# Kernel tuning notes

Measured on AMD Instinct MI355X. Metric: run time of the kernel, lower is better.

## Reference

```python
import jax, jax.numpy as jnp
import numpy as np

V, D, H, L = 50000, 50, 50, 100   # vocab, input_dim, hidden_dim, latent_dim
WIN = 5
B = 65536
MARGIN = 1.0


def setup_inputs() -> dict:
    key = jax.random.key(0)
    ks = jax.random.split(key, 12)
    emb = jax.random.normal(ks[0], (V, D), jnp.float32) * 0.1
    emb = emb.at[0].set(0.0)  # padding_idx=0
    W1 = jax.random.normal(ks[1], (2 * D, H), jnp.float32) * 0.1
    b1 = jnp.zeros((H,), jnp.float32)
    Wmu = jax.random.normal(ks[2], (H, L), jnp.float32) * 0.1
    bmu = jnp.zeros((L,), jnp.float32)
    Wls = jax.random.normal(ks[3], (H, 1), jnp.float32) * 0.1
    bls = jnp.zeros((1,), jnp.float32)
    type_means_tbl = jax.random.normal(ks[4], (V, L), jnp.float32) * 0.1
    type_logvars_tbl = jax.random.normal(ks[5], (V, 1), jnp.float32) * 0.1
    centers = jax.random.randint(ks[6], (B,), 1, V, jnp.int32)
    contexts = jax.random.randint(ks[7], (B, 2 * WIN), 1, V, jnp.int32)
    neg_contexts = jax.random.randint(ks[8], (B, 2 * WIN), 1, V, jnp.int32)
    return {"emb": emb, "W1": W1, "b1": b1, "Wmu": Wmu, "bmu": bmu,
            "Wls": Wls, "bls": bls, "type_means_tbl": type_means_tbl,
            "type_logvars_tbl": type_logvars_tbl, "centers": centers,
            "contexts": contexts, "neg_contexts": neg_contexts}


def _kl(idx, post_mu, post_logsigma, type_means_tbl, type_logvars_tbl):
    # idx: [N] int; post_mu: [N,L]; post_logsigma: [N,1]
    post_sigma = jnp.exp(post_logsigma)                      # [N,1]
    type_mean = type_means_tbl[idx]                          # [N,L]
    type_logvar = type_logvars_tbl[idx]                      # [N,1]
    type_var = jnp.exp(type_logvar)                          # [N,1]
    var_division = post_sigma / type_var                     # [N,1]
    diff = post_mu - type_mean                               # [N,L]
    diff_term = jnp.sum(diff * diff, axis=1, keepdims=True) / type_var  # [N,1]
    logvar_division = type_logvar - post_logsigma            # [N,1]
    return 0.5 * ((var_division + diff_term + logvar_division)[:, 0] - L)  # [N]


def reference(emb, W1, b1, Wmu, bmu, Wls, bls, type_means_tbl, type_logvars_tbl,
              centers, contexts, neg_contexts):
    Bn, C = contexts.shape                                   # C = 2*window
    e_ctx = emb[contexts]                                    # [B,C,D]
    e_cen = emb[centers]                                     # [B,D]
    # concat(context_embed, center_repeat) along feature dim -> [B,C,2D]
    cat = jnp.concatenate(
        [e_ctx, jnp.broadcast_to(e_cen[:, None, :], (Bn, C, D))], axis=-1)
    h = jax.nn.relu(jnp.einsum('bcf,fh->bch', cat, W1) + b1).sum(axis=1)  # [B,H]
    mu = h @ Wmu + bmu                                       # [B,L]
    logsigma = h @ Wls + bls                                 # [B,1]
    # repeat each row 2*window times (matches repeat(1,2w).view(-1,L))
    mus = jnp.repeat(mu, C, axis=0)                          # [B*C,L]
    logsigmas = jnp.repeat(logsigma, C, axis=0)              # [B*C,1]
    kl_ctx = _kl(contexts.reshape(-1), mus, logsigmas, type_means_tbl, type_logvars_tbl)
    kl_neg = _kl(neg_contexts.reshape(-1), mus, logsigmas, type_means_tbl, type_logvars_tbl)
    kl_cen = _kl(centers, mu, logsigma, type_means_tbl, type_logvars_tbl)
    hinge = jnp.maximum(kl_ctx - kl_neg + MARGIN, 0.0)
    loss = hinge.sum() + kl_cen.sum()
    return loss / Bn
```

## Files before the change

### kernel.cpp

```cpp
#include <hip/hip_runtime.h>

namespace {
constexpr int V    = 50000;
constexpr int D    = 50;
constexpr int H    = 50;
constexpr int LDIM = 100;
constexpr int C    = 10;
constexpr int B    = 65536;
constexpr int NTILES = B / 16;

constexpr size_t OFF_EMB  = 0;
constexpr size_t OFF_TM   = OFF_EMB + (size_t)V * 64 * 2;
constexpr size_t OFF_W1T  = OFF_TM + (size_t)V * 128;
constexpr size_t OFF_W1B  = OFF_W1T + 2 * 4 * 64 * 8 * 2;
constexpr size_t OFF_WMU  = OFF_W1B + 2 * 4 * 64 * 8 * 2;
constexpr size_t OFF_B1P  = OFF_WMU + 2 * 7 * 64 * 8 * 2;
constexpr size_t OFF_BMUP = OFF_B1P + 64 * 4;
constexpr size_t OFF_WLSP = OFF_BMUP + 128 * 4;
constexpr size_t OFF_TT   = OFF_WLSP + 64 * 4;
constexpr size_t OFF_MUF  = OFF_TT + (size_t)V * 16;
constexpr size_t OFF_MSL  = OFF_MUF + (size_t)NTILES * 4 * 64 * 8;
constexpr size_t OFF_PART = OFF_MSL + (size_t)B * 16;
constexpr size_t WS_NEED  = OFF_PART + (size_t)NTILES * 4;

typedef __attribute__((ext_vector_type(8))) short short8;
typedef __attribute__((ext_vector_type(4))) float f32x4;
typedef unsigned long long ull;

__device__ __forceinline__ unsigned short f2bf(float x) {
  unsigned u = __builtin_bit_cast(unsigned, x);
  unsigned r = (u + 0x7FFFu + ((u >> 16) & 1u)) >> 16;
  return (unsigned short)r;
}

__global__ __launch_bounds__(256) void bsg_prep(
    const float* __restrict__ emb, const float* __restrict__ tm,
    const float* __restrict__ tlv, const float* __restrict__ W1,
    const float* __restrict__ Wmu, const float* __restrict__ b1,
    const float* __restrict__ bmu, const float* __restrict__ Wls,
    unsigned short* __restrict__ embB, unsigned char* __restrict__ tmF8,
    float4* __restrict__ tt4, unsigned short* __restrict__ w1t,
    unsigned short* __restrict__ w1b, unsigned short* __restrict__ wmuB,
    float* __restrict__ b1p, float* __restrict__ bmup, float* __restrict__ wlsp) {
  const int EMB_T = V * 8;
  const int TM_T  = V * 8;
  const int stride = gridDim.x * blockDim.x;
  for (int t = blockIdx.x * blockDim.x + threadIdx.x; t < EMB_T + TM_T; t += stride) {
    if (t < EMB_T) {
      int v = t >> 3, c = t & 7, k0 = c * 8;
      unsigned short r[8];
#pragma unroll
      for (int e = 0; e < 8; ++e) {
        int k = k0 + e;
        r[e] = f2bf(k < D ? emb[(size_t)v * D + k] : 0.f);
      }
      uint4 o;
      o.x = (unsigned)r[0] | ((unsigned)r[1] << 16);
      o.y = (unsigned)r[2] | ((unsigned)r[3] << 16);
      o.z = (unsigned)r[4] | ((unsigned)r[5] << 16);
      o.w = (unsigned)r[6] | ((unsigned)r[7] << 16);
      ((uint4*)(embB + (size_t)v * 64))[c] = o;
    } else {
      int t2 = t - EMB_T;
      int v = t2 >> 3, c = t2 & 7, k0 = c * 16;
      float val[16];
#pragma unroll
      for (int e = 0; e < 16; ++e) {
        int k = k0 + e;
        val[e] = (k < LDIM) ? tm[(size_t)v * LDIM + k] : 0.f;
      }
      uint4 o;
      unsigned dw[4];
      float sq = 0.f;
#pragma unroll
      for (int j = 0; j < 4; ++j) {
        int d = __builtin_amdgcn_cvt_pk_fp8_f32(val[4 * j + 0], val[4 * j + 1], 0, false);
        d = __builtin_amdgcn_cvt_pk_fp8_f32(val[4 * j + 2], val[4 * j + 3], d, true);
        dw[j] = (unsigned)d;
        float q0 = __builtin_amdgcn_cvt_f32_fp8(d, 0);
        float q1 = __builtin_amdgcn_cvt_f32_fp8(d, 1);
        float q2 = __builtin_amdgcn_cvt_f32_fp8(d, 2);
        float q3 = __builtin_amdgcn_cvt_f32_fp8(d, 3);
        sq = fmaf(q0, q0, sq); sq = fmaf(q1, q1, sq);
        sq = fmaf(q2, q2, sq); sq = fmaf(q3, q3, sq);
      }
      o.x = dw[0]; o.y = dw[1]; o.z = dw[2]; o.w = dw[3];
      ((uint4*)(tmF8 + (size_t)v * 128))[c] = o;
#pragma unroll
      for (int off = 1; off < 8; off <<= 1) sq += __shfl_xor(sq, off);
      if (c == 0) {
        float tl = tlv[v];
        float4 q;
        q.x = tl; q.y = __expf(-tl); q.z = sq; q.w = 0.f;
        tt4[v] = q;
      }
    }
  }
  if (blockIdx.x == 0) {
    const int tid = threadIdx.x;
    for (int id = tid; id < 1024; id += 256) {
      int half = id >> 9, rem = id & 511;
      int ks = rem >> 8, nt = (rem >> 6) & 3, l = rem & 63;
      unsigned short r[8];
      int n = nt * 16 + (l & 15);
#pragma unroll
      for (int e = 0; e < 8; ++e) {
        int f = ks * 32 + ((l >> 4) << 3) + e;
        float v = (f < D && n < H) ? W1[(size_t)(half * D + f) * H + n] : 0.f;
        r[e] = f2bf(v);
      }
      uint4 o;
      o.x = (unsigned)r[0] | ((unsigned)r[1] << 16);
      o.y = (unsigned)r[2] | ((unsigned)r[3] << 16);
      o.z = (unsigned)r[4] | ((unsigned)r[5] << 16);
      o.w = (unsigned)r[6] | ((unsigned)r[7] << 16);
      unsigned short* dst = half ? w1b : w1t;
      ((uint4*)dst)[(ks * 4 + nt) * 64 + l] = o;
    }
    for (int id = tid; id < 896; id += 256) {
      int ks = id / 448, rem = id % 448;
      int nt = rem >> 6, l = rem & 63;
      unsigned short r[8];
      int n = nt * 16 + (l & 15);
#pragma unroll
      for (int e = 0; e < 8; ++e) {
        int j = ks * 32 + ((l >> 4) << 3) + e;
        float v = (j < H && n < LDIM) ? Wmu[(size_t)j * LDIM + n] : 0.f;
        r[e] = f2bf(v);
      }
      uint4 o;
      o.x = (unsigned)r[0] | ((unsigned)r[1] << 16);
      o.y = (unsigned)r[2] | ((unsigned)r[3] << 16);
      o.z = (unsigned)r[4] | ((unsigned)r[5] << 16);
      o.w = (unsigned)r[6] | ((unsigned)r[7] << 16);
      ((uint4*)wmuB)[(ks * 7 + nt) * 64 + l] = o;
    }
    if (tid < 64)  b1p[tid]  = (tid < H)    ? b1[tid]  : 0.f;
    if (tid < 128) bmup[tid] = (tid < LDIM) ? bmu[tid] : 0.f;
    if (tid < 64)  wlsp[tid] = (tid < H)    ? Wls[tid] : 0.f;
  }
}

__global__ __launch_bounds__(256, 4) void bsg_mlp(
    const unsigned short* __restrict__ embB,
    const unsigned short* __restrict__ w1t,
    const unsigned short* __restrict__ w1b,
    const unsigned short* __restrict__ wmuB,
    const float* __restrict__ b1p, const float* __restrict__ bmup,
    const float* __restrict__ wlsp, const float* __restrict__ bls,
    const int* __restrict__ centers, const int* __restrict__ contexts,
    ull* __restrict__ muF, float4* __restrict__ msl) {
  __shared__ unsigned short hlds[32][64];
  __shared__ unsigned char kb[2][16][128];
  __shared__ float logsp[2][32];
  __shared__ float musq_p[2][2][16];

  const int tid = threadIdx.x;
  const int w = tid >> 6, l = tid & 63;
  const int srow = l & 15, kc = l >> 4;
  const int st = w & 1, np = w >> 1;
  const int sblk = blockIdx.x * 32;
  const int sg = sblk + st * 16 + srow;

  char* kbbase = (char*)&kb[0][0][0];
  auto kb_ptr = [&](int st_, int s_, int kbyte) -> char* {
    return kbbase + st_ * 2048 + s_ * 128 + (kbyte ^ ((s_ & 7) << 4));
  };

  {
    int st_ = tid >> 7, rem = tid & 127;
    int s_ = rem >> 3, j = rem & 7;
    *(unsigned short*)kb_ptr(st_, s_, 112 + 2 * j) = 0;
  }

  int cen = centers[sg];
  int cidx[10];
#pragma unroll
  for (int c = 0; c < 10; ++c) cidx[c] = contexts[sg * 10 + c];

  const short8* w1tF = (const short8*)w1t;
  const short8* w1bF = (const short8*)w1b;

  short8 Bz[2][2], Bt[2][2];
#pragma unroll
  for (int n2 = 0; n2 < 2; ++n2)
#pragma unroll
    for (int ks = 0; ks < 2; ++ks) {
      Bz[n2][ks] = w1bF[(ks * 4 + 2 * np + n2) * 64 + l];
      Bt[n2][ks] = w1tF[(ks * 4 + 2 * np + n2) * 64 + l];
    }

  const short8* Ace = (const short8*)(embB + (size_t)cen * 64);
  short8 Ac0 = Ace[kc], Ac1 = Ace[4 + kc];
  f32x4 Z[2] = {{0.f, 0.f, 0.f, 0.f}, {0.f, 0.f, 0.f, 0.f}};
#pragma unroll
  for (int n2 = 0; n2 < 2; ++n2) {
    Z[n2] = __builtin_amdgcn_mfma_f32_16x16x32_bf16(Ac0, Bz[n2][0], Z[n2], 0, 0, 0);
    Z[n2] = __builtin_amdgcn_mfma_f32_16x16x32_bf16(Ac1, Bz[n2][1], Z[n2], 0, 0, 0);
  }
  float b1v[2] = {b1p[(2 * np + 0) * 16 + srow], b1p[(2 * np + 1) * 16 + srow]};

  f32x4 hv[2] = {{0.f, 0.f, 0.f, 0.f}, {0.f, 0.f, 0.f, 0.f}};
  for (int c = 0; c < 10; ++c) {
    const short8* Ar = (const short8*)(embB + (size_t)cidx[c] * 64);
    short8 A0 = Ar[kc], A1 = Ar[4 + kc];
#pragma unroll
    for (int n2 = 0; n2 < 2; ++n2) {
      f32x4 acc = {0.f, 0.f, 0.f, 0.f};
      acc = __builtin_amdgcn_mfma_f32_16x16x32_bf16(A0, Bt[n2][0], acc, 0, 0, 0);
      acc = __builtin_amdgcn_mfma_f32_16x16x32_bf16(A1, Bt[n2][1], acc, 0, 0, 0);
#pragma unroll
      for (int q = 0; q < 4; ++q)
        hv[n2][q] += fmaxf(acc[q] + Z[n2][q] + b1v[n2], 0.f);
    }
  }
  {
    float wl0 = wlsp[(2 * np + 0) * 16 + srow];
    float wl1 = wlsp[(2 * np + 1) * 16 + srow];
    float lp[4];
#pragma unroll
    for (int q = 0; q < 4; ++q) lp[q] = hv[0][q] * wl0 + hv[1][q] * wl1;
#pragma unroll
    for (int off = 1; off < 16; off <<= 1)
#pragma unroll
      for (int q = 0; q < 4; ++q) lp[q] += __shfl_xor(lp[q], off);
    if (srow == 0) {
#pragma unroll
      for (int q = 0; q < 4; ++q) logsp[np][st * 16 + kc * 4 + q] = lp[q];
    }
  }
#pragma unroll
  for (int n2 = 0; n2 < 2; ++n2)
#pragma unroll
    for (int q = 0; q < 4; ++q)
      hlds[st * 16 + kc * 4 + q][(2 * np + n2) * 16 + srow] = f2bf(hv[n2][q]);
  __syncthreads();

  {
    const short8* hrow = (const short8*)&hlds[st * 16 + srow][0];
    short8 Ah0 = hrow[kc], Ah1 = hrow[4 + kc];
    const short8* wmF = (const short8*)wmuB;
    f32x4 sqv = {0.f, 0.f, 0.f, 0.f};
    for (int nt = np; nt < 7; nt += 2) {
      short8 B0 = wmF[(0 * 7 + nt) * 64 + l];
      short8 B1 = wmF[(1 * 7 + nt) * 64 + l];
      f32x4 m = {0.f, 0.f, 0.f, 0.f};
      m = __builtin_amdgcn_mfma_f32_16x16x32_bf16(Ah0, B0, m, 0, 0, 0);
      m = __builtin_amdgcn_mfma_f32_16x16x32_bf16(Ah1, B1, m, 0, 0, 0);
      int lcol = nt * 16 + srow;
      float bm = bmup[lcol];
      float mv0 = m[0] + bm, mv1 = m[1] + bm, mv2 = m[2] + bm, mv3 = m[3] + bm;
      int d01 = __builtin_amdgcn_cvt_pk_fp8_f32(mv0, mv1, 0, false);
      int d23 = __builtin_amdgcn_cvt_pk_fp8_f32(mv2, mv3, 0, false);
      float q0 = __builtin_amdgcn_cvt_f32_fp8(d01, 0);
      float q1 = __builtin_amdgcn_cvt_f32_fp8(d01, 1);
      float q2 = __builtin_amdgcn_cvt_f32_fp8(d23, 0);
      float q3 = __builtin_amdgcn_cvt_f32_fp8(d23, 1);
      sqv[0] = fmaf(q0, q0, sqv[0]);
      sqv[1] = fmaf(q1, q1, sqv[1]);
      sqv[2] = fmaf(q2, q2, sqv[2]);
      sqv[3] = fmaf(q3, q3, sqv[3]);
      *(unsigned char*)kb_ptr(st, kc * 4 + 0, lcol) = (unsigned char)(d01 & 0xFF);
      *(unsigned char*)kb_ptr(st, kc * 4 + 1, lcol) = (unsigned char)((d01 >> 8) & 0xFF);
      *(unsigned char*)kb_ptr(st, kc * 4 + 2, lcol) = (unsigned char)(d23 & 0xFF);
      *(unsigned char*)kb_ptr(st, kc * 4 + 3, lcol) = (unsigned char)((d23 >> 8) & 0xFF);
    }
#pragma unroll
    for (int off = 1; off < 16; off <<= 1)
#pragma unroll
      for (int q = 0; q < 4; ++q) sqv[q] += __shfl_xor(sqv[q], off);
    if (srow == 0) {
#pragma unroll
      for (int q = 0; q < 4; ++q) musq_p[np][st][kc * 4 + q] = sqv[q];
    }
  }
  __syncthreads();

  if (w < 2) {
    size_t gt = (size_t)blockIdx.x * 2 + w;
#pragma unroll
    for (int ks = 0; ks < 4; ++ks) {
      ull v = *(const ull*)kb_ptr(w, srow, ks * 32 + kc * 8);
      muF[(gt * 4 + ks) * 64 + l] = v;
    }
  } else if (w == 2 && l < 32) {
    int s_ = l;
    float lg = bls[0] + logsp[0][s_] + logsp[1][s_];
    float msq = musq_p[0][s_ >> 4][s_ & 15] + musq_p[1][s_ >> 4][s_ & 15];
    float4 o;
    o.x = lg; o.y = __expf(lg); o.z = msq; o.w = 0.f;
    msl[sblk + s_] = o;
  }
}

__global__ __launch_bounds__(256) void bsg_kl(
    const unsigned char* __restrict__ tmF8, const float4* __restrict__ tt4,
    const ull* __restrict__ muF, const float4* __restrict__ msl,
    const int* __restrict__ centers, const int* __restrict__ contexts,
    const int* __restrict__ negctx, float* __restrict__ partials) {
  __shared__ char klds[4][4 * 2048];

  const int w = threadIdx.x >> 6, l = threadIdx.x & 63;
  const int gt = blockIdx.x * 4 + w;
  const int srow = l & 15, kc = l >> 4;
  const int s = gt * 16 + srow;
  const int s3 = srow & 3;

  char* myl = &klds[w][0];
  const int cofs = ((kc ^ s3) << 4);
  const int rA = ((((kc >> 1) ^ s3) * 16 + srow) * 16) + (kc & 1) * 8;
  const int rB = ((((2 + (kc >> 1)) ^ s3) * 16 + srow) * 16) + (kc & 1) * 8;

  ull Bmu[4];
#pragma unroll
  for (int ks = 0; ks < 4; ++ks) Bmu[ks] = muF[((size_t)gt * 4 + ks) * 64 + l];

  const float4 m = msl[s];
  const float lg = m.x, ps = m.y, msq = m.z;
  const bool isdiag = (kc == (srow >> 2));
  const int qd = srow & 3;

  int idx[21];
  idx[0] = centers[s];
#pragma unroll
  for (int c = 0; c < 10; ++c) idx[1 + c] = contexts[s * 10 + c];
#pragma unroll
  for (int c = 0; c < 10; ++c) idx[11 + c] = negctx[s * 10 + c];

  constexpr int ord[21] = {0, 1, 11, 2, 12, 3, 13, 4, 14, 5, 15,
                           6, 16, 7, 17, 8, 18, 9, 19, 10, 20};

  float4 ttb[4];
  float loss = 0.f, klc = 0.f;

#define KL_STAGE(T)                                                          \
  do {                                                                       \
    const unsigned char* src_ = tmF8 + (size_t)idx[ord[(T)]] * 128 + cofs;   \
    char* d0_ = myl + ((T) & 3) * 2048;                                      \
    __builtin_amdgcn_global_load_lds(                                        \
        (const __attribute__((address_space(1))) unsigned int*)src_,         \
        (__attribute__((address_space(3))) unsigned int*)d0_, 16, 0, 0);     \
    __builtin_amdgcn_global_load_lds(                                        \
        (const __attribute__((address_space(1))) unsigned int*)(src_ + 64),  \
        (__attribute__((address_space(3))) unsigned int*)(d0_ + 1024),       \
        16, 0, 0);                                                           \
    ttb[(T) & 3] = tt4[idx[ord[(T)]]];                                       \
  } while (0)

#define KL_STEP(T, NW)                                                       \
  do {                                                                       \
    if ((T) + 3 < 21) KL_STAGE((T) + 3);                                     \
    asm volatile("s_waitcnt vmcnt(" #NW ")" ::: "memory");                   \
    __builtin_amdgcn_sched_barrier(0);                                       \
    const char* kb_ = myl + ((T) & 3) * 2048;                                \
    ull a0_ = *(const ull*)(kb_ + rA);                                       \
    ull a1_ = *(const ull*)(kb_ + rB);                                       \
    ull a2_ = *(const ull*)(kb_ + rA + 1024);                                \
    ull a3_ = *(const ull*)(kb_ + rB + 1024);                                \
    f32x4 acc_ = {0.f, 0.f, 0.f, 0.f};                                       \
    acc_ = __builtin_amdgcn_mfma_f32_16x16x32_fp8_fp8((long)a0_, (long)Bmu[0], acc_, 0, 0, 0); \
    acc_ = __builtin_amdgcn_mfma_f32_16x16x32_fp8_fp8((long)a1_, (long)Bmu[1], acc_, 0, 0, 0); \
    acc_ = __builtin_amdgcn_mfma_f32_16x16x32_fp8_fp8((long)a2_, (long)Bmu[2], acc_, 0, 0, 0); \
    acc_ = __builtin_amdgcn_mfma_f32_16x16x32_fp8_fp8((long)a3_, (long)Bmu[3], acc_, 0, 0, 0); \
    float4 tv_ = ttb[(T) & 3];                                               \
    float dot_ = (qd & 2) ? ((qd & 1) ? acc_[3] : acc_[2])                   \
                          : ((qd & 1) ? acc_[1] : acc_[0]);                  \
    float dsum_ = msq + tv_.z - 2.f * dot_;                                  \
    float kl_ = 0.5f * (fmaf(ps + dsum_, tv_.y, tv_.x - lg) - (float)LDIM);  \
    if ((T) == 0)      loss += isdiag ? kl_ : 0.f;                           \
    else if ((T) & 1)  klc = kl_;                                            \
    else               loss += isdiag ? fmaxf(klc - kl_ + 1.f, 0.f) : 0.f;   \
  } while (0)

  KL_STAGE(0);
  KL_STAGE(1);
  KL_STAGE(2);

  KL_STEP(0, 6);  KL_STEP(1, 6);  KL_STEP(2, 6);  KL_STEP(3, 6);
  KL_STEP(4, 6);  KL_STEP(5, 6);  KL_STEP(6, 6);  KL_STEP(7, 6);
  KL_STEP(8, 6);  KL_STEP(9, 6);  KL_STEP(10, 6); KL_STEP(11, 6);
  KL_STEP(12, 6); KL_STEP(13, 6); KL_STEP(14, 6); KL_STEP(15, 6);
  KL_STEP(16, 6); KL_STEP(17, 6); KL_STEP(18, 4); KL_STEP(19, 2);
  KL_STEP(20, 0);

#undef KL_STEP
#undef KL_STAGE

#pragma unroll
  for (int off = 32; off > 0; off >>= 1) loss += __shfl_down(loss, off);
  if (l == 0) partials[gt] = loss;
}

__global__ __launch_bounds__(256) void bsg_reduce(const float* __restrict__ partials,
                                                  int n, float* __restrict__ out) {
  double v = 0.0;
  for (int i = threadIdx.x; i < n; i += 256) v += (double)partials[i];
#pragma unroll
  for (int off = 32; off > 0; off >>= 1) v += __shfl_down(v, off);
  __shared__ double ws4[4];
  if ((threadIdx.x & 63) == 0) ws4[threadIdx.x >> 6] = v;
  __syncthreads();
  if (threadIdx.x == 0) {
    double t = 0.0;
#pragma unroll
    for (int k = 0; k < 4; ++k) t += ws4[k];
    out[0] = (float)(t / (double)B);
  }
}

__device__ __forceinline__ float kl_term_fb(const float* mu, float ps, float logs,
                                            int idx, const float* tm_tbl,
                                            const float* tlv_tbl) {
  const float* tm = tm_tbl + (size_t)idx * LDIM;
  float tlv = tlv_tbl[idx];
  float d0 = 0.f, d1 = 0.f, d2 = 0.f, d3 = 0.f;
#pragma unroll
  for (int l = 0; l < LDIM; l += 4) {
    float4 t = *reinterpret_cast<const float4*>(tm + l);
    float a0 = mu[l] - t.x, a1 = mu[l + 1] - t.y;
    float a2 = mu[l + 2] - t.z, a3 = mu[l + 3] - t.w;
    d0 = fmaf(a0, a0, d0); d1 = fmaf(a1, a1, d1);
    d2 = fmaf(a2, a2, d2); d3 = fmaf(a3, a3, d3);
  }
  return 0.5f * (fmaf(ps + (d0 + d1) + (d2 + d3), __expf(-tlv), tlv - logs) - (float)LDIM);
}

__global__ __launch_bounds__(256) void bsg_fb(
    const float* __restrict__ emb, const float* __restrict__ W1,
    const float* __restrict__ b1, const float* __restrict__ Wmu,
    const float* __restrict__ bmu, const float* __restrict__ Wls,
    const float* __restrict__ bls, const float* __restrict__ tm_tbl,
    const float* __restrict__ tlv_tbl, const int* __restrict__ centers,
    const int* __restrict__ contexts, const int* __restrict__ negctx,
    float* __restrict__ partials) {
  const int b = blockIdx.x * 256 + threadIdx.x;
  const int cen = centers[b];
  float ecen[D];
  const float* ep = emb + (size_t)cen * D;
#pragma unroll
  for (int f = 0; f < D; f += 2) {
    float2 v = *reinterpret_cast<const float2*>(ep + f);
    ecen[f] = v.x; ecen[f + 1] = v.y;
  }
  float z[H];
#pragma unroll
  for (int j = 0; j < H; ++j) z[j] = b1[j];
#pragma unroll
  for (int f = 0; f < D; ++f) {
    float vf = ecen[f];
#pragma unroll
    for (int j = 0; j < H; ++j) z[j] = fmaf(vf, W1[(D + f) * H + j], z[j]);
  }
  float h[H];
#pragma unroll
  for (int j = 0; j < H; ++j) h[j] = 0.f;
  for (int c = 0; c < C; ++c) {
    const float* ecp = emb + (size_t)contexts[b * C + c] * D;
    float s[H];
#pragma unroll
    for (int j = 0; j < H; ++j) s[j] = z[j];
#pragma unroll
    for (int f = 0; f < D; ++f) {
      float vf = ecp[f];
#pragma unroll
      for (int j = 0; j < H; ++j) s[j] = fmaf(vf, W1[f * H + j], s[j]);
    }
#pragma unroll
    for (int j = 0; j < H; ++j) h[j] += fmaxf(s[j], 0.f);
  }
  float mu[LDIM];
#pragma unroll
  for (int l = 0; l < LDIM; ++l) mu[l] = bmu[l];
#pragma unroll
  for (int j = 0; j < H; ++j) {
    float hj = h[j];
#pragma unroll
    for (int l = 0; l < LDIM; ++l) mu[l] = fmaf(hj, Wmu[j * LDIM + l], mu[l]);
  }
  float logs = bls[0];
#pragma unroll
  for (int j = 0; j < H; ++j) logs = fmaf(h[j], Wls[j], logs);
  float ps = __expf(logs);
  float acc = kl_term_fb(mu, ps, logs, cen, tm_tbl, tlv_tbl);
  for (int c = 0; c < C; ++c) {
    float kc = kl_term_fb(mu, ps, logs, contexts[b * C + c], tm_tbl, tlv_tbl);
    float kn = kl_term_fb(mu, ps, logs, negctx[b * C + c], tm_tbl, tlv_tbl);
    acc += fmaxf(kc - kn + 1.f, 0.f);
  }
  float vs = acc;
#pragma unroll
  for (int off = 32; off > 0; off >>= 1) vs += __shfl_down(vs, off);
  __shared__ float wsum[4];
  if ((threadIdx.x & 63) == 0) wsum[threadIdx.x >> 6] = vs;
  __syncthreads();
  if (threadIdx.x == 0) {
    float t = 0.f;
#pragma unroll
    for (int k = 0; k < 4; ++k) t += wsum[k];
    partials[blockIdx.x] = t;
  }
}
}

extern "C" void kernel_launch(void* const* d_in, const int* in_sizes, int n_in,
                              void* d_out, int out_size, void* d_ws, size_t ws_size,
                              hipStream_t stream) {
  const float* emb     = (const float*)d_in[0];
  const float* W1      = (const float*)d_in[1];
  const float* b1      = (const float*)d_in[2];
  const float* Wmu     = (const float*)d_in[3];
  const float* bmu     = (const float*)d_in[4];
  const float* Wls     = (const float*)d_in[5];
  const float* bls     = (const float*)d_in[6];
  const float* tm      = (const float*)d_in[7];
  const float* tlv     = (const float*)d_in[8];
  const int*   centers = (const int*)d_in[9];
  const int*   ctx     = (const int*)d_in[10];
  const int*   negc    = (const int*)d_in[11];
  float* out = (float*)d_out;

  if (ws_size < WS_NEED + 1024) {
    float* partials = (float*)d_ws;
    bsg_fb<<<256, 256, 0, stream>>>(emb, W1, b1, Wmu, bmu, Wls, bls, tm, tlv,
                                    centers, ctx, negc, partials);
    bsg_reduce<<<1, 256, 0, stream>>>(partials, 256, out);
    return;
  }

  char* ws = (char*)d_ws;
  unsigned short* embB = (unsigned short*)(ws + OFF_EMB);
  unsigned char*  tmF8 = (unsigned char*)(ws + OFF_TM);
  unsigned short* w1t  = (unsigned short*)(ws + OFF_W1T);
  unsigned short* w1b  = (unsigned short*)(ws + OFF_W1B);
  unsigned short* wmuB = (unsigned short*)(ws + OFF_WMU);
  float* b1p  = (float*)(ws + OFF_B1P);
  float* bmup = (float*)(ws + OFF_BMUP);
  float* wlsp = (float*)(ws + OFF_WLSP);
  float4* tt4 = (float4*)(ws + OFF_TT);
  ull* muF    = (ull*)(ws + OFF_MUF);
  float4* msl = (float4*)(ws + OFF_MSL);
  float* partials = (float*)(ws + OFF_PART);

  bsg_prep<<<1024, 256, 0, stream>>>(emb, tm, tlv, W1, Wmu, b1, bmu, Wls,
                                     embB, tmF8, tt4, w1t, w1b, wmuB, b1p, bmup, wlsp);
  bsg_mlp<<<B / 32, 256, 0, stream>>>(embB, w1t, w1b, wmuB, b1p, bmup, wlsp, bls,
                                      centers, ctx, muF, msl);
  bsg_kl<<<NTILES / 4, 256, 0, stream>>>(tmF8, tt4, muF, msl, centers, ctx, negc,
                                         partials);
  bsg_reduce<<<1, 256, 0, stream>>>(partials, NTILES, out);
}
```

Measured before the change: 79.68 us.

## Pipeline embedding gathers through LDS with async global_load_lds ring buffer

Embedding row gathers for the center and ten context words now go through a four-deep per-wave LDS ring filled by asynchronous global_load_lds. Loads are issued three steps ahead, and explicit vmcnt waits let the MFMA work overlap with gather latency. The LDS reads use an XOR swizzle, and launch bounds drop from 4 to 3 blocks per SM to make room for the 32KB staging buffer. The cost is more LDS per block and lower occupancy, which may offset the latency hiding.

```diff
diff --git a/kernel.cpp b/kernel.cpp
--- a/kernel.cpp
+++ b/kernel.cpp
@@ -141,7 +141,7 @@
   }
 }
 
-__global__ __launch_bounds__(256, 4) void bsg_mlp(
+__global__ __launch_bounds__(256, 3) void bsg_mlp(
     const unsigned short* __restrict__ embB,
     const unsigned short* __restrict__ w1t,
     const unsigned short* __restrict__ w1b,
@@ -154,6 +154,7 @@
   __shared__ unsigned char kb[2][16][128];
   __shared__ float logsp[2][32];
   __shared__ float musq_p[2][2][16];
+  __shared__ char stg[4][4 * 2048];
 
   const int tid = threadIdx.x;
   const int w = tid >> 6, l = tid & 63;
@@ -161,6 +162,7 @@
   const int st = w & 1, np = w >> 1;
   const int sblk = blockIdx.x * 32;
   const int sg = sblk + st * 16 + srow;
+  const int s3 = srow & 3;
 
   char* kbbase = (char*)&kb[0][0][0];
   auto kb_ptr = [&](int st_, int s_, int kbyte) -> char* {
@@ -173,10 +175,14 @@
     *(unsigned short*)kb_ptr(st_, s_, 112 + 2 * j) = 0;
   }
 
-  int cen = centers[sg];
-  int cidx[10];
-#pragma unroll
-  for (int c = 0; c < 10; ++c) cidx[c] = contexts[sg * 10 + c];
+  char* myl = &stg[w][0];
+  const int cofs = ((kc ^ s3) << 4);
+  const int aoff = ((kc ^ s3) << 8) + (srow << 4);
+
+  int rid[11];
+  rid[0] = centers[sg];
+#pragma unroll
+  for (int c = 0; c < 10; ++c) rid[1 + c] = contexts[sg * 10 + c];
 
   const short8* w1tF = (const short8*)w1t;
   const short8* w1bF = (const short8*)w1b;
@@ -189,37 +195,70 @@
       Bz[n2][ks] = w1bF[(ks * 4 + 2 * np + n2) * 64 + l];
       Bt[n2][ks] = w1tF[(ks * 4 + 2 * np + n2) * 64 + l];
     }
-
-  const short8* Ace = (const short8*)(embB + (size_t)cen * 64);
-  short8 Ac0 = Ace[kc], Ac1 = Ace[4 + kc];
-  f32x4 Z[2] = {{0.f, 0.f, 0.f, 0.f}, {0.f, 0.f, 0.f, 0.f}};
-#pragma unroll
-  for (int n2 = 0; n2 < 2; ++n2) {
-    Z[n2] = __builtin_amdgcn_mfma_f32_16x16x32_bf16(Ac0, Bz[n2][0], Z[n2], 0, 0, 0);
-    Z[n2] = __builtin_amdgcn_mfma_f32_16x16x32_bf16(Ac1, Bz[n2][1], Z[n2], 0, 0, 0);
-  }
   float b1v[2] = {b1p[(2 * np + 0) * 16 + srow], b1p[(2 * np + 1) * 16 + srow]};
 
-  f32x4 hv[2] = {{0.f, 0.f, 0.f, 0.f}, {0.f, 0.f, 0.f, 0.f}};
-  for (int c = 0; c < 10; ++c) {
-    const short8* Ar = (const short8*)(embB + (size_t)cidx[c] * 64);
-    short8 A0 = Ar[kc], A1 = Ar[4 + kc];
-#pragma unroll
-    for (int n2 = 0; n2 < 2; ++n2) {
-      f32x4 acc = {0.f, 0.f, 0.f, 0.f};
-      acc = __builtin_amdgcn_mfma_f32_16x16x32_bf16(A0, Bt[n2][0], acc, 0, 0, 0);
-      acc = __builtin_amdgcn_mfma_f32_16x16x32_bf16(A1, Bt[n2][1], acc, 0, 0, 0);
-#pragma unroll
-      for (int q = 0; q < 4; ++q)
-        hv[n2][q] += fmaxf(acc[q] + Z[n2][q] + b1v[n2], 0.f);
-    }
-  }
+  const unsigned char* embBy = (const unsigned char*)embB;
+
+  f32x4 Z0 = {0.f, 0.f, 0.f, 0.f}, Z1 = {0.f, 0.f, 0.f, 0.f};
+  f32x4 hv0 = {0.f, 0.f, 0.f, 0.f}, hv1 = {0.f, 0.f, 0.f, 0.f};
+
+#define MLP_STAGE(T)                                                         \
+  do {                                                                       \
+    const unsigned char* src_ = embBy + (size_t)rid[(T)] * 128 + cofs;       \
+    char* d0_ = myl + ((T) & 3) * 2048;                                      \
+    __builtin_amdgcn_global_load_lds(                                        \
+        (const __attribute__((address_space(1))) unsigned int*)src_,         \
+        (__attribute__((address_space(3))) unsigned int*)d0_, 16, 0, 0);     \
+    __builtin_amdgcn_global_load_lds(                                        \
+        (const __attribute__((address_space(1))) unsigned int*)(src_ + 64),  \
+        (__attribute__((address_space(3))) unsigned int*)(d0_ + 1024),       \
+        16, 0, 0);                                                           \
+  } while (0)
+
+#define MLP_STEP(T, NW)                                                      \
+  do {                                                                       \
+    if ((T) + 3 < 11) MLP_STAGE((T) + 3);                                    \
+    asm volatile("s_waitcnt vmcnt(" #NW ")" ::: "memory");                   \
+    __builtin_amdgcn_sched_barrier(0);                                       \
+    const char* sb_ = myl + ((T) & 3) * 2048;                                \
+    short8 A0_ = *(const short8*)(sb_ + aoff);                               \
+    short8 A1_ = *(const short8*)(sb_ + 1024 + aoff);                        \
+    if ((T) == 0) {                                                          \
+      Z0 = __builtin_amdgcn_mfma_f32_16x16x32_bf16(A0_, Bz[0][0], Z0, 0, 0, 0); \
+      Z0 = __builtin_amdgcn_mfma_f32_16x16x32_bf16(A1_, Bz[0][1], Z0, 0, 0, 0); \
+      Z1 = __builtin_amdgcn_mfma_f32_16x16x32_bf16(A0_, Bz[1][0], Z1, 0, 0, 0); \
+      Z1 = __builtin_amdgcn_mfma_f32_16x16x32_bf16(A1_, Bz[1][1], Z1, 0, 0, 0); \
+    } else {                                                                 \
+      f32x4 ac0_ = {0.f, 0.f, 0.f, 0.f}, ac1_ = {0.f, 0.f, 0.f, 0.f};        \
+      ac0_ = __builtin_amdgcn_mfma_f32_16x16x32_bf16(A0_, Bt[0][0], ac0_, 0, 0, 0); \
+      ac0_ = __builtin_amdgcn_mfma_f32_16x16x32_bf16(A1_, Bt[0][1], ac0_, 0, 0, 0); \
+      ac1_ = __builtin_amdgcn_mfma_f32_16x16x32_bf16(A0_, Bt[1][0], ac1_, 0, 0, 0); \
+      ac1_ = __builtin_amdgcn_mfma_f32_16x16x32_bf16(A1_, Bt[1][1], ac1_, 0, 0, 0); \
+      _Pragma("unroll")                                                      \
+      for (int q = 0; q < 4; ++q) {                                          \
+        hv0[q] += fmaxf(ac0_[q] + Z0[q] + b1v[0], 0.f);                      \
+        hv1[q] += fmaxf(ac1_[q] + Z1[q] + b1v[1], 0.f);                      \
+      }                                                                      \
+    }                                                                        \
+  } while (0)
+
+  MLP_STAGE(0);
+  MLP_STAGE(1);
+  MLP_STAGE(2);
+
+  MLP_STEP(0, 6); MLP_STEP(1, 6); MLP_STEP(2, 6); MLP_STEP(3, 6);
+  MLP_STEP(4, 6); MLP_STEP(5, 6); MLP_STEP(6, 6); MLP_STEP(7, 6);
+  MLP_STEP(8, 4); MLP_STEP(9, 2); MLP_STEP(10, 0);
+
+#undef MLP_STEP
+#undef MLP_STAGE
+
   {
     float wl0 = wlsp[(2 * np + 0) * 16 + srow];
     float wl1 = wlsp[(2 * np + 1) * 16 + srow];
     float lp[4];
 #pragma unroll
-    for (int q = 0; q < 4; ++q) lp[q] = hv[0][q] * wl0 + hv[1][q] * wl1;
+    for (int q = 0; q < 4; ++q) lp[q] = hv0[q] * wl0 + hv1[q] * wl1;
 #pragma unroll
     for (int off = 1; off < 16; off <<= 1)
 #pragma unroll
@@ -230,10 +269,10 @@
     }
   }
 #pragma unroll
-  for (int n2 = 0; n2 < 2; ++n2)
-#pragma unroll
-    for (int q = 0; q < 4; ++q)
-      hlds[st * 16 + kc * 4 + q][(2 * np + n2) * 16 + srow] = f2bf(hv[n2][q]);
+  for (int q = 0; q < 4; ++q) {
+    hlds[st * 16 + kc * 4 + q][(2 * np + 0) * 16 + srow] = f2bf(hv0[q]);
+    hlds[st * 16 + kc * 4 + q][(2 * np + 1) * 16 + srow] = f2bf(hv1[q]);
+  }
   __syncthreads();
 
   {
```

Measured after the change: 76.27 us. 4.3% less time.
